# Performance work log

Measured on AMD Instinct MI355X. Metric: run time of the kernel, lower is better.

The kernel has to match this reference:

```python
import jax, jax.numpy as jnp
import numpy as np

K = 20          # n_neighbors
EPS = 1e-5      # batchnorm eps
SLOPE = 0.2     # leaky relu slope (DGCNN default)


def _bn_lrelu(x, axes):
    # batch-norm (per-batch stats, gamma=1, beta=0) + LeakyReLU(0.2)
    m = jnp.mean(x, axis=axes, keepdims=True)
    v = jnp.var(x, axis=axes, keepdims=True)
    return jax.nn.leaky_relu((x - m) * jax.lax.rsqrt(v + EPS), SLOPE)


def _knn(x_cf, k):
    # x_cf: (B, C, N) -> idx (B, N, k) of k nearest neighbors (incl. self)
    inner = jnp.einsum('bcn,bcm->bnm', x_cf, x_cf)
    sq = jnp.sum(x_cf * x_cf, axis=1)                  # (B, N)
    neg_d = 2.0 * inner - sq[:, :, None] - sq[:, None, :]
    return jax.lax.top_k(neg_d, k)[1]


def _gather(x_nl, idx):
    # x_nl: (B, N, C), idx: (B, N, k) -> (B, N, k, C) neighbor features
    return jnp.take_along_axis(x_nl[:, :, None, :], idx[..., None], axis=1)


def setup_inputs() -> dict:
    key = jax.random.key(0)
    ks = jax.random.split(key, 11)
    B, N, C = 16, 2048, 3
    dims = [64, 64, 128, 256]
    feat_dim = 1024

    def w(k, o, i):
        return jax.random.normal(k, (o, i), jnp.float32) / np.sqrt(i)

    return {
        'x': jax.random.normal(ks[0], (B, N, C), jnp.float32),
        'w_edge': w(ks[1], dims[0], 2 * C),
        'b_edge': jnp.zeros((dims[0],), jnp.float32),
        'w1': w(ks[2], dims[1], dims[0]),
        'b1': jnp.zeros((dims[1],), jnp.float32),
        'w2': w(ks[3], dims[2], dims[1]),
        'b2': jnp.zeros((dims[2],), jnp.float32),
        'w3': w(ks[4], dims[3], dims[2]),
        'b3': jnp.zeros((dims[3],), jnp.float32),
        'w_final': w(ks[5], feat_dim, sum(dims)),
        'b_final': jnp.zeros((feat_dim,), jnp.float32),
    }


def reference(x, w_edge, b_edge, w1, b1, w2, b2, w3, b3, w_final, b_final):
    # x: (B, N, 3) point cloud
    x_cf = jnp.transpose(x, (0, 2, 1))                 # (B, 3, N)
    idx = _knn(x_cf, K)                                # (B, N, k) -- graph built once

    # get_graph_features: edge feature = concat(neighbor - center, center)
    nb = _gather(x, idx)                               # (B, N, k, 3)
    ctr = jnp.broadcast_to(x[:, :, None, :], nb.shape)
    feat = jnp.concatenate([nb - ctr, ctr], axis=-1)   # (B, N, k, 6)

    # EdgeConvLayer: 1x1 conv2d + BN + LeakyReLU, then max over neighbors
    h = jnp.einsum('oc,bnkc->bonk', w_edge, feat) + b_edge[None, :, None, None]
    h = _bn_lrelu(h, (0, 2, 3))
    h = jnp.max(h, axis=3)                             # (B, 64, N)

    xs = [h]
    for w, b in ((w1, b1), (w2, b2), (w3, b3)):
        # graph_max_pooling with reused kNN indices
        g = jnp.max(_gather(jnp.transpose(h, (0, 2, 1)), idx), axis=2)  # (B, N, C)
        h = jnp.einsum('oc,bnc->bon', w, g) + b[None, :, None]          # 1x1 conv1d
        h = _bn_lrelu(h, (0, 2))
        xs.append(h)

    h_cat = jnp.concatenate(xs, axis=1)                # (B, 512, N)
    out = jnp.einsum('oc,bcn->bon', w_final, h_cat) + b_final[None, :, None]
    return jnp.max(out, axis=2)                        # (B, 1024)
```

## Files before the change

### kernel.cpp

```cpp
#include <hip/hip_runtime.h>
#include <hip/hip_bf16.h>
#include <math.h>

#define B_ 16
#define N_ 2048
#define KNN 20
#define SLOPE 0.2f
#define EPS_ 1e-5f

#define SEG 8
#define SEGLEN (N_ / SEG)
#define QPB 64
#define CAP 64

typedef __attribute__((ext_vector_type(8))) short short8;
typedef __attribute__((ext_vector_type(4))) float float4v;

__global__ __launch_bounds__(256, 2) void knn_kernel(const float* __restrict__ x,
                                                     int* __restrict__ idx) {
    __shared__ float4 pts4[N_];
    __shared__ float thr[QPB * 24];
    __shared__ float tq[QPB];
    __shared__ int cnt[QPB];
    __shared__ float lv[QPB * CAP];
    __shared__ int   li[QPB * CAP];

    const int b = blockIdx.x >> 5;
    const int qb = blockIdx.x & 31;
    const float* xb = x + (size_t)b * N_ * 3;
    for (int i = threadIdx.x; i < N_; i += 256) {
        float xv = xb[i * 3], yv = xb[i * 3 + 1], zv = xb[i * 3 + 2];
        pts4[i] = make_float4(xv, yv, zv, xv * xv + yv * yv + zv * zv);
    }
    if (threadIdx.x < QPB) cnt[threadIdx.x] = 0;
    __syncthreads();

    const int s = threadIdx.x >> 5;
    const int qs = threadIdx.x & 31;
    const int q0 = qs * 2, q1 = q0 + 1;
    const int n0 = qb * QPB + q0;
    const float4 pa = pts4[n0];
    const float4 pb = pts4[n0 + 1];
    const int m0 = s * SEGLEN;
    const int rot = s * 9;

    float ca[8], cb[8];
#pragma unroll
    for (int c = 0; c < 8; ++c) {
        float va = -INFINITY, vb = -INFINITY;
        for (int i = 0; i < 32; ++i) {
            const int m = m0 + ((c * 32 + i + rot) & (SEGLEN - 1));
            const float4 p = pts4[m];
            va = fmaxf(va, 2.f * (pa.x * p.x + pa.y * p.y + pa.z * p.z) - pa.w - p.w);
            vb = fmaxf(vb, 2.f * (pb.x * p.x + pb.y * p.y + pb.z * p.z) - pb.w - p.w);
        }
        ca[c] = va; cb[c] = vb;
    }
    {
        float t0 = -INFINITY, t1 = -INFINITY, t2 = -INFINITY;
        float u0 = -INFINITY, u1 = -INFINITY, u2 = -INFINITY;
#pragma unroll
        for (int c = 0; c < 8; ++c) {
            float v = ca[c];
            float r0 = fminf(t0, v); t0 = fmaxf(t0, v);
            float r1 = fminf(t1, r0); t1 = fmaxf(t1, r0);
            t2 = fmaxf(t2, r1);
            float w = cb[c];
            float s0 = fminf(u0, w); u0 = fmaxf(u0, w);
            float s1 = fminf(u1, s0); u1 = fmaxf(u1, s0);
            u2 = fmaxf(u2, s1);
        }
        thr[q0 * 24 + s * 3 + 0] = t0;
        thr[q0 * 24 + s * 3 + 1] = t1;
        thr[q0 * 24 + s * 3 + 2] = t2;
        thr[q1 * 24 + s * 3 + 0] = u0;
        thr[q1 * 24 + s * 3 + 1] = u1;
        thr[q1 * 24 + s * 3 + 2] = u2;
    }
    __syncthreads();

    if (threadIdx.x < QPB) {
        const int qq = threadIdx.x;
        float s0 = INFINITY, s1 = INFINITY, s2 = INFINITY, s3 = INFINITY, s4 = INFINITY;
#pragma unroll
        for (int j = 0; j < 24; ++j) {
            float c = thr[qq * 24 + j];
            float u;
            u = fminf(s0, c); c = fmaxf(s0, c); s0 = u;
            u = fminf(s1, c); c = fmaxf(s1, c); s1 = u;
            u = fminf(s2, c); c = fmaxf(s2, c); s2 = u;
            u = fminf(s3, c); c = fmaxf(s3, c); s3 = u;
            s4 = fminf(s4, c);
        }
        tq[qq] = s4 - (fabsf(s4) * 1e-6f + 1e-6f);
    }
    __syncthreads();

    const float ta = tq[q0];
    const float tb = tq[q1];
    for (int i = 0; i < SEGLEN; ++i) {
        const int m = m0 + ((i + rot) & (SEGLEN - 1));
        const float4 p = pts4[m];
        const float da = 2.f * (pa.x * p.x + pa.y * p.y + pa.z * p.z) - pa.w - p.w;
        const float db = 2.f * (pb.x * p.x + pb.y * p.y + pb.z * p.z) - pb.w - p.w;
        if (da >= ta) {
            int pos = atomicAdd(&cnt[q0], 1);
            if (pos < CAP) { lv[q0 * CAP + pos] = da; li[q0 * CAP + pos] = m; }
        }
        if (db >= tb) {
            int pos = atomicAdd(&cnt[q1], 1);
            if (pos < CAP) { lv[q1 * CAP + pos] = db; li[q1 * CAP + pos] = m; }
        }
    }
    __syncthreads();

    if (threadIdx.x < QPB) {
        const int qq = threadIdx.x;
        const int nn = qb * QPB + qq;
        int* op = idx + (size_t)(b * N_ + nn) * KNN;
        float vals[KNN]; int inds[KNN];
#pragma unroll
        for (int j = 0; j < KNN; ++j) { vals[j] = -INFINITY; inds[j] = 0; }
        const int c = cnt[qq];
        if (c <= CAP) {
            for (int j = 0; j < c; ++j) {
                const float v = lv[qq * CAP + j];
                if (v > vals[KNN - 1]) {
                    float cv = v; int ci = li[qq * CAP + j];
#pragma unroll
                    for (int k = 0; k < KNN; ++k) {
                        const bool sw = cv > vals[k];
                        const float tv = vals[k]; const int ti = inds[k];
                        vals[k] = sw ? cv : tv;  inds[k] = sw ? ci : ti;
                        cv      = sw ? tv : cv;  ci      = sw ? ti : ci;
                    }
                }
            }
        } else {
            const float4 pq2 = pts4[nn];
            for (int m = 0; m < N_; ++m) {
                const float4 p = pts4[m];
                const float d = 2.f * (pq2.x * p.x + pq2.y * p.y + pq2.z * p.z)
                                - pq2.w - p.w;
                if (d > vals[KNN - 1]) {
                    float cv = d; int ci = m;
#pragma unroll
                    for (int k = 0; k < KNN; ++k) {
                        const bool sw = cv > vals[k];
                        const float tv = vals[k]; const int ti = inds[k];
                        vals[k] = sw ? cv : tv;  inds[k] = sw ? ci : ti;
                        cv      = sw ? tv : cv;  ci      = sw ? ti : ci;
                    }
                }
            }
        }
#pragma unroll
        for (int j = 0; j < KNN; ++j) op[j] = inds[j];
    }
}

__global__ __launch_bounds__(256) void edge_kernel(const float* __restrict__ x,
                                                   const int* __restrict__ idx,
                                                   const float* __restrict__ w_edge,
                                                   const float* __restrict__ b_edge,
                                                   float* __restrict__ cat,
                                                   double* __restrict__ stats) {
    __shared__ float xs[N_ * 3];
    __shared__ float ws[64 * 6];
    __shared__ float bs[64];
    __shared__ float s_sum[64], s_sq[64];

    int b = blockIdx.x >> 5;
    int pb = blockIdx.x & 31;
    const float* xb = x + (size_t)b * N_ * 3;
    for (int i = threadIdx.x; i < N_ * 3; i += 256) xs[i] = xb[i];
    for (int i = threadIdx.x; i < 64 * 6; i += 256) ws[i] = w_edge[i];
    if (threadIdx.x < 64) {
        bs[threadIdx.x] = b_edge[threadIdx.x];
        s_sum[threadIdx.x] = 0.f; s_sq[threadIdx.x] = 0.f;
    }
    __syncthreads();

    int p = threadIdx.x >> 2;
    int cg = threadIdx.x & 3;
    int n = pb * 64 + p;
    float cx = xs[n * 3], cy = xs[n * 3 + 1], cz = xs[n * 3 + 2];

    float maxv[16], sum[16], sq[16];
#pragma unroll
    for (int i = 0; i < 16; ++i) { maxv[i] = -INFINITY; sum[i] = 0.f; sq[i] = 0.f; }

    const int* ip = idx + (size_t)(b * N_ + n) * KNN;
    for (int k = 0; k < KNN; ++k) {
        int j = ip[k];
        float dx = xs[j * 3] - cx, dy = xs[j * 3 + 1] - cy, dz = xs[j * 3 + 2] - cz;
#pragma unroll
        for (int i = 0; i < 16; ++i) {
            int o = cg * 16 + i;
            const float* wr = &ws[o * 6];
            float h = bs[o] + wr[0] * dx + wr[1] * dy + wr[2] * dz
                            + wr[3] * cx + wr[4] * cy + wr[5] * cz;
            sum[i] += h; sq[i] += h * h;
            maxv[i] = fmaxf(maxv[i], h);
        }
    }

    float* cp = cat + (size_t)(b * N_ + n) * 512;
#pragma unroll
    for (int i = 0; i < 16; ++i) {
        int o = cg * 16 + i;
        cp[o] = maxv[i];
        atomicAdd(&s_sum[o], sum[i]);
        atomicAdd(&s_sq[o], sq[i]);
    }
    __syncthreads();
    if (threadIdx.x < 64) {
        atomicAdd(&stats[threadIdx.x], (double)s_sum[threadIdx.x]);
        atomicAdd(&stats[64 + threadIdx.x], (double)s_sq[threadIdx.x]);
    }
}

__global__ __launch_bounds__(256) void bn_kernel(float* __restrict__ cat,
                                                 __hip_bfloat16* __restrict__ catb,
                                                 const double* __restrict__ stats,
                                                 int C, int off, double invcnt) {
    int t = blockIdx.x * 256 + threadIdx.x;
    int c = t % C;
    int pn = t / C;
    double meand = stats[c] * invcnt;
    double ex2 = stats[C + c] * invcnt;
    float var = (float)(ex2 - meand * meand);
    float mean = (float)meand;
    float inv = rsqrtf(var + EPS_);
    size_t o = (size_t)pn * 512 + off + c;
    float v = (cat[o] - mean) * inv;
    v = v >= 0.f ? v : SLOPE * v;
    cat[o] = v;
    if (catb) catb[o] = __float2bfloat16(v);
}

__global__ __launch_bounds__(256) void wconv_kernel(const float* __restrict__ w,
                                                    __hip_bfloat16* __restrict__ wb) {
    int t = blockIdx.x * 256 + threadIdx.x;
    wb[t] = __float2bfloat16(w[t]);
}

template <int CIN, int COUT, int P, int PT>
__global__ __launch_bounds__(256) void layer_kernel(float* __restrict__ cat,
                                                    const int* __restrict__ idx,
                                                    const float* __restrict__ w,
                                                    const float* __restrict__ bias,
                                                    double* __restrict__ stats,
                                                    int off_in, int off_out) {
    constexpr int LDC = CIN + 4;
    constexpr int WS = COUT + 4;
    constexpr int NCG = CIN / 4;
    constexpr int PPAR = 256 / NCG;
    constexpr int NOG = COUT / 4;

    __shared__ float g[P * LDC];
    __shared__ float wt[16 * WS];
    __shared__ float s_sum[COUT], s_sq[COUT];

    const int pt0 = blockIdx.x * P;
    const int b = pt0 / N_;

    {
        const int cg = threadIdx.x % NCG;
        const int pp = threadIdx.x / NCG;
        for (int p = pp; p < P; p += PPAR) {
            const int* ip = idx + (size_t)(pt0 + p) * KNN;
            float4 m = make_float4(-INFINITY, -INFINITY, -INFINITY, -INFINITY);
#pragma unroll
            for (int k = 0; k < KNN; ++k) {
                const int j = ip[k];
                const float4 v = *(const float4*)&cat[(size_t)(b * N_ + j) * 512 + off_in + cg * 4];
                m.x = fmaxf(m.x, v.x); m.y = fmaxf(m.y, v.y);
                m.z = fmaxf(m.z, v.z); m.w = fmaxf(m.w, v.w);
            }
            *(float4*)&g[p * LDC + cg * 4] = m;
        }
    }
    if (threadIdx.x < COUT) { s_sum[threadIdx.x] = 0.f; s_sq[threadIdx.x] = 0.f; }

    const int og = threadIdx.x % NOG;
    const int pg = threadIdx.x / NOG;
    const int o0 = og * 4, p0 = pg * PT;

    float acc[4][PT];
#pragma unroll
    for (int i = 0; i < 4; ++i)
#pragma unroll
        for (int j = 0; j < PT; ++j) acc[i][j] = 0.f;

    for (int c0 = 0; c0 < CIN; c0 += 16) {
        __syncthreads();
        for (int i = threadIdx.x; i < COUT * 16; i += 256) {
            int o = i >> 4, cc = i & 15;
            wt[cc * WS + o] = w[(size_t)o * CIN + c0 + cc];
        }
        __syncthreads();
#pragma unroll
        for (int cc = 0; cc < 16; ++cc) {
            const float4 wv = *(const float4*)&wt[cc * WS + o0];
            const float* gp = &g[p0 * LDC + c0 + cc];
#pragma unroll
            for (int p = 0; p < PT; ++p) {
                const float gv = gp[p * LDC];
                acc[0][p] += wv.x * gv;
                acc[1][p] += wv.y * gv;
                acc[2][p] += wv.z * gv;
                acc[3][p] += wv.w * gv;
            }
        }
    }

    const float4 bv = *(const float4*)&bias[o0];
    float lsum[4] = {0.f, 0.f, 0.f, 0.f}, lsq[4] = {0.f, 0.f, 0.f, 0.f};
#pragma unroll
    for (int p = 0; p < PT; ++p) {
        float4 hv;
        hv.x = acc[0][p] + bv.x; hv.y = acc[1][p] + bv.y;
        hv.z = acc[2][p] + bv.z; hv.w = acc[3][p] + bv.w;
        lsum[0] += hv.x; lsq[0] += hv.x * hv.x;
        lsum[1] += hv.y; lsq[1] += hv.y * hv.y;
        lsum[2] += hv.z; lsq[2] += hv.z * hv.z;
        lsum[3] += hv.w; lsq[3] += hv.w * hv.w;
        *(float4*)&cat[(size_t)(pt0 + p0 + p) * 512 + off_out + o0] = hv;
    }
#pragma unroll
    for (int i = 0; i < 4; ++i) {
        atomicAdd(&s_sum[o0 + i], lsum[i]);
        atomicAdd(&s_sq[o0 + i], lsq[i]);
    }
    __syncthreads();
    if (threadIdx.x < COUT) {
        atomicAdd(&stats[threadIdx.x], (double)s_sum[threadIdx.x]);
        atomicAdd(&stats[COUT + threadIdx.x], (double)s_sq[threadIdx.x]);
    }
}

__global__ __launch_bounds__(256) void final_mfma_kernel(const short* __restrict__ catb,
                                                         const short* __restrict__ wb,
                                                         const float* __restrict__ bias,
                                                         float* __restrict__ partial) {
    constexpr int LDK = 72;
    __shared__ short As[128 * LDK];
    __shared__ short Bs[128 * LDK];
    __shared__ float red[256];

    const int ob = blockIdx.x;
    const int pblk = blockIdx.y;
    const int pt0 = pblk * 128;

    const int wid = threadIdx.x >> 6;
    const int lane = threadIdx.x & 63;
    const int wm = wid >> 1, wn = wid & 1;
    const int lm = lane & 15, g = lane >> 4;

    const int srow = threadIdx.x >> 1;
    const int scg = (threadIdx.x & 1) * 32;
    const short* ga = catb + (size_t)(pt0 + srow) * 512 + scg;
    const short* gb = wb + (size_t)(ob * 128 + srow) * 512 + scg;
    short* la = As + srow * LDK + scg;
    short* lb = Bs + srow * LDK + scg;

    float4v acc[4][4];
#pragma unroll
    for (int i = 0; i < 4; ++i)
#pragma unroll
        for (int j = 0; j < 4; ++j) acc[i][j] = {0.f, 0.f, 0.f, 0.f};

    short8 ra[4], rb[4];
#pragma unroll
    for (int j = 0; j < 4; ++j) {
        ra[j] = *(const short8*)(ga + j * 8);
        rb[j] = *(const short8*)(gb + j * 8);
    }

    for (int step = 0; step < 8; ++step) {
        __syncthreads();
#pragma unroll
        for (int j = 0; j < 4; ++j) {
            *(short8*)(la + j * 8) = ra[j];
            *(short8*)(lb + j * 8) = rb[j];
        }
        __syncthreads();
        if (step < 7) {
            const int c1 = (step + 1) * 64;
#pragma unroll
            for (int j = 0; j < 4; ++j) {
                ra[j] = *(const short8*)(ga + c1 + j * 8);
                rb[j] = *(const short8*)(gb + c1 + j * 8);
            }
        }
#pragma unroll
        for (int kk = 0; kk < 2; ++kk) {
            short8 a[4], b[4];
#pragma unroll
            for (int t = 0; t < 4; ++t) {
                a[t] = *(const short8*)&As[(wm * 64 + t * 16 + lm) * LDK + kk * 32 + g * 8];
                b[t] = *(const short8*)&Bs[(wn * 64 + t * 16 + lm) * LDK + kk * 32 + g * 8];
            }
#pragma unroll
            for (int mt = 0; mt < 4; ++mt)
#pragma unroll
                for (int nt = 0; nt < 4; ++nt)
                    acc[mt][nt] = __builtin_amdgcn_mfma_f32_16x16x32_bf16(
                        a[mt], b[nt], acc[mt][nt], 0, 0, 0);
        }
    }

    float cm[4];
#pragma unroll
    for (int nt = 0; nt < 4; ++nt) {
        float m = -INFINITY;
#pragma unroll
        for (int mt = 0; mt < 4; ++mt)
#pragma unroll
            for (int r = 0; r < 4; ++r) m = fmaxf(m, acc[mt][nt][r]);
        m = fmaxf(m, __shfl_xor(m, 16, 64));
        m = fmaxf(m, __shfl_xor(m, 32, 64));
        cm[nt] = m;
    }
    __syncthreads();
    if (lane < 16) {
#pragma unroll
        for (int nt = 0; nt < 4; ++nt)
            red[wm * 128 + wn * 64 + nt * 16 + lane] = cm[nt];
    }
    __syncthreads();
    if (threadIdx.x < 128) {
        const int o = threadIdx.x;
        float v = fmaxf(red[o], red[128 + o]) + bias[ob * 128 + o];
        partial[(size_t)pblk * 1024 + ob * 128 + o] = v;
    }
}

__global__ __launch_bounds__(256) void final_kernel(const float* __restrict__ cat,
                                                    const float* __restrict__ w,
                                                    const float* __restrict__ bias,
                                                    float* __restrict__ partial) {
    __shared__ float As[16 * 132];
    __shared__ float Ws[16 * 132];
    __shared__ float red[16 * 128];

    const int ob = blockIdx.x;
    const int pblk = blockIdx.y;
    const int pt0 = pblk * 128;
    const int tx = threadIdx.x & 15;
    const int ty = threadIdx.x >> 4;

    float acc[8][8];
#pragma unroll
    for (int i = 0; i < 8; ++i)
#pragma unroll
        for (int j = 0; j < 8; ++j) acc[i][j] = 0.f;

    const int row = threadIdx.x & 127;
    const int half = threadIdx.x >> 7;
    const float* arow = cat + (size_t)(pt0 + row) * 512 + half * 8;
    const float* wrow = w + (size_t)(ob * 128 + row) * 512 + half * 8;

    for (int c0 = 0; c0 < 512; c0 += 16) {
        __syncthreads();
        float4 v0 = *(const float4*)(arow + c0);
        float4 v1 = *(const float4*)(arow + c0 + 4);
        float4 u0 = *(const float4*)(wrow + c0);
        float4 u1 = *(const float4*)(wrow + c0 + 4);
        const int cb = half * 8;
        As[(cb + 0) * 132 + row] = v0.x; As[(cb + 1) * 132 + row] = v0.y;
        As[(cb + 2) * 132 + row] = v0.z; As[(cb + 3) * 132 + row] = v0.w;
        As[(cb + 4) * 132 + row] = v1.x; As[(cb + 5) * 132 + row] = v1.y;
        As[(cb + 6) * 132 + row] = v1.z; As[(cb + 7) * 132 + row] = v1.w;
        Ws[(cb + 0) * 132 + row] = u0.x; Ws[(cb + 1) * 132 + row] = u0.y;
        Ws[(cb + 2) * 132 + row] = u0.z; Ws[(cb + 3) * 132 + row] = u0.w;
        Ws[(cb + 4) * 132 + row] = u1.x; Ws[(cb + 5) * 132 + row] = u1.y;
        Ws[(cb + 6) * 132 + row] = u1.z; Ws[(cb + 7) * 132 + row] = u1.w;
        __syncthreads();
#pragma unroll
        for (int cc = 0; cc < 16; ++cc) {
            const float4* Ap = (const float4*)(As + cc * 132);
            const float4* Wp = (const float4*)(Ws + cc * 132);
            float4 a0 = Ap[ty], a1 = Ap[ty + 16];
            float4 w0 = Wp[tx], w1 = Wp[tx + 16];
            float av[8] = {a0.x, a0.y, a0.z, a0.w, a1.x, a1.y, a1.z, a1.w};
            float wv[8] = {w0.x, w0.y, w0.z, w0.w, w1.x, w1.y, w1.z, w1.w};
#pragma unroll
            for (int i = 0; i < 8; ++i)
#pragma unroll
                for (int j = 0; j < 8; ++j)
                    acc[i][j] += av[i] * wv[j];
        }
    }

#pragma unroll
    for (int j = 0; j < 8; ++j) {
        float mm = acc[0][j];
#pragma unroll
        for (int i = 1; i < 8; ++i) mm = fmaxf(mm, acc[i][j]);
        const int o = (j < 4) ? tx * 4 + j : 64 + tx * 4 + (j - 4);
        red[ty * 128 + o] = mm;
    }
    __syncthreads();
    if (threadIdx.x < 128) {
        const int o = threadIdx.x;
        float mm = red[o];
#pragma unroll
        for (int r = 1; r < 16; ++r) mm = fmaxf(mm, red[r * 128 + o]);
        partial[(size_t)pblk * 1024 + ob * 128 + o] = mm + bias[ob * 128 + o];
    }
}

__global__ __launch_bounds__(256) void reduce_kernel(const float* __restrict__ partial,
                                                     float* __restrict__ out) {
    int t = blockIdx.x * 256 + threadIdx.x;
    int b = t >> 10, o = t & 1023;
    float m = -INFINITY;
#pragma unroll 4
    for (int i = 0; i < 16; ++i)
        m = fmaxf(m, partial[(size_t)((b * 16 + i) * 1024) + o]);
    out[t] = m;
}

extern "C" void kernel_launch(void* const* d_in, const int* in_sizes, int n_in,
                              void* d_out, int out_size, void* d_ws, size_t ws_size,
                              hipStream_t stream) {
    const float* x = (const float*)d_in[0];
    const float* w_edge = (const float*)d_in[1];
    const float* b_edge = (const float*)d_in[2];
    const float* w1 = (const float*)d_in[3];
    const float* b1 = (const float*)d_in[4];
    const float* w2 = (const float*)d_in[5];
    const float* b2 = (const float*)d_in[6];
    const float* w3 = (const float*)d_in[7];
    const float* b3 = (const float*)d_in[8];
    const float* w_final = (const float*)d_in[9];
    const float* b_final = (const float*)d_in[10];
    float* out = (float*)d_out;

    char* ws = (char*)d_ws;
    int* idx = (int*)ws;
    float* cat = (float*)(ws + 2621440);
    float* partial = (float*)(ws + 69730304);
    double* stats = (double*)(ws + 70778880);
    __hip_bfloat16* catb = (__hip_bfloat16*)(ws + 70787072);
    __hip_bfloat16* wb = (__hip_bfloat16*)(ws + 104341504);
    const size_t WS_NEED = 105390080;
    const bool use_mfma = (ws_size >= WS_NEED);
    __hip_bfloat16* catb_arg = use_mfma ? catb : (__hip_bfloat16*)0;

    double* st_e = stats;
    double* st_1 = stats + 128;
    double* st_2 = stats + 256;
    double* st_3 = stats + 512;

    hipMemsetAsync(stats, 0, 1024 * sizeof(double), stream);
    if (use_mfma)
        wconv_kernel<<<2048, 256, 0, stream>>>(w_final, wb);

    knn_kernel<<<B_ * 32, 256, 0, stream>>>(x, idx);
    edge_kernel<<<B_ * 32, 256, 0, stream>>>(x, idx, w_edge, b_edge, cat, st_e);
    bn_kernel<<<(B_ * N_ * 64) / 256, 256, 0, stream>>>(cat, catb_arg, st_e, 64, 0,
                                                        1.0 / ((double)B_ * N_ * KNN));
    layer_kernel<64, 64, 64, 4><<<(B_ * N_) / 64, 256, 0, stream>>>(cat, idx, w1, b1, st_1, 0, 64);
    bn_kernel<<<(B_ * N_ * 64) / 256, 256, 0, stream>>>(cat, catb_arg, st_1, 64, 64,
                                                        1.0 / ((double)B_ * N_));
    layer_kernel<64, 128, 64, 8><<<(B_ * N_) / 64, 256, 0, stream>>>(cat, idx, w2, b2, st_2, 64, 128);
    bn_kernel<<<(B_ * N_ * 128) / 256, 256, 0, stream>>>(cat, catb_arg, st_2, 128, 128,
                                                         1.0 / ((double)B_ * N_));
    layer_kernel<128, 256, 64, 16><<<(B_ * N_) / 64, 256, 0, stream>>>(cat, idx, w3, b3, st_3, 128, 256);
    bn_kernel<<<(B_ * N_ * 256) / 256, 256, 0, stream>>>(cat, catb_arg, st_3, 256, 256,
                                                         1.0 / ((double)B_ * N_));
    if (use_mfma)
        final_mfma_kernel<<<dim3(8, 256), 256, 0, stream>>>((const short*)catb, (const short*)wb,
                                                            b_final, partial);
    else
        final_kernel<<<dim3(8, 256), 256, 0, stream>>>(cat, w_final, b_final, partial);
    reduce_kernel<<<64, 256, 0, stream>>>(partial, out);
}
```

Before: 437.3 us.

## Fuse BN+LeakyReLU into neighbor gather and consolidate BN into single bf16 pass

Removes the four separate bn_kernel passes. Each layer now applies the previous layer's batch-norm and LeakyReLU while it gathers and max-pools neighbor features. This is valid because the transform is monotonic per channel, so it commutes with max. A single bnconv_kernel then normalizes the whole 512-channel concat buffer to bf16 for the MFMA final GEMM. It also changes the layer's weight smem layout to per-output rows with float4 reads over input channels, drops the rotated scan order in kNN, and removes the fp32 fallback final kernel. The goal is to cut global read/write traffic and launch count, at the cost of a workspace-size check and possible LDS bank conflicts.

```diff
diff --git a/kernel.cpp b/kernel.cpp
--- a/kernel.cpp
+++ b/kernel.cpp
@@ -42,14 +42,13 @@
     const float4 pa = pts4[n0];
     const float4 pb = pts4[n0 + 1];
     const int m0 = s * SEGLEN;
-    const int rot = s * 9;
 
     float ca[8], cb[8];
 #pragma unroll
     for (int c = 0; c < 8; ++c) {
         float va = -INFINITY, vb = -INFINITY;
         for (int i = 0; i < 32; ++i) {
-            const int m = m0 + ((c * 32 + i + rot) & (SEGLEN - 1));
+            const int m = m0 + c * 32 + i;
             const float4 p = pts4[m];
             va = fmaxf(va, 2.f * (pa.x * p.x + pa.y * p.y + pa.z * p.z) - pa.w - p.w);
             vb = fmaxf(vb, 2.f * (pb.x * p.x + pb.y * p.y + pb.z * p.z) - pb.w - p.w);
@@ -99,7 +98,7 @@
     const float ta = tq[q0];
     const float tb = tq[q1];
     for (int i = 0; i < SEGLEN; ++i) {
-        const int m = m0 + ((i + rot) & (SEGLEN - 1));
+        const int m = m0 + i;
         const float4 p = pts4[m];
         const float da = 2.f * (pa.x * p.x + pa.y * p.y + pa.z * p.z) - pa.w - p.w;
         const float db = 2.f * (pb.x * p.x + pb.y * p.y + pb.z * p.z) - pb.w - p.w;
@@ -220,46 +219,30 @@
     }
 }
 
-__global__ __launch_bounds__(256) void bn_kernel(float* __restrict__ cat,
-                                                 __hip_bfloat16* __restrict__ catb,
-                                                 const double* __restrict__ stats,
-                                                 int C, int off, double invcnt) {
-    int t = blockIdx.x * 256 + threadIdx.x;
-    int c = t % C;
-    int pn = t / C;
-    double meand = stats[c] * invcnt;
-    double ex2 = stats[C + c] * invcnt;
-    float var = (float)(ex2 - meand * meand);
-    float mean = (float)meand;
-    float inv = rsqrtf(var + EPS_);
-    size_t o = (size_t)pn * 512 + off + c;
-    float v = (cat[o] - mean) * inv;
-    v = v >= 0.f ? v : SLOPE * v;
-    cat[o] = v;
-    if (catb) catb[o] = __float2bfloat16(v);
-}
-
 __global__ __launch_bounds__(256) void wconv_kernel(const float* __restrict__ w,
                                                     __hip_bfloat16* __restrict__ wb) {
     int t = blockIdx.x * 256 + threadIdx.x;
     wb[t] = __float2bfloat16(w[t]);
 }
 
-template <int CIN, int COUT, int P, int PT>
+template <int CIN, int COUT, int PT>
 __global__ __launch_bounds__(256) void layer_kernel(float* __restrict__ cat,
                                                     const int* __restrict__ idx,
                                                     const float* __restrict__ w,
                                                     const float* __restrict__ bias,
-                                                    double* __restrict__ stats,
+                                                    const double* __restrict__ stats_in,
+                                                    double invcnt_in,
+                                                    double* __restrict__ stats_out,
                                                     int off_in, int off_out) {
+    constexpr int P = 64;
     constexpr int LDC = CIN + 4;
-    constexpr int WS = COUT + 4;
     constexpr int NCG = CIN / 4;
     constexpr int PPAR = 256 / NCG;
     constexpr int NOG = COUT / 4;
+    static_assert(NOG * (P / PT) == 256, "thread mapping");
 
     __shared__ float g[P * LDC];
-    __shared__ float wt[16 * WS];
+    __shared__ float wt[COUT * 20];
     __shared__ float s_sum[COUT], s_sq[COUT];
 
     const int pt0 = blockIdx.x * P;
@@ -268,6 +251,15 @@
     {
         const int cg = threadIdx.x % NCG;
         const int pp = threadIdx.x / NCG;
+        float mean[4], inv[4];
+#pragma unroll
+        for (int j = 0; j < 4; ++j) {
+            const double mu = stats_in[cg * 4 + j] * invcnt_in;
+            const double e2 = stats_in[CIN + cg * 4 + j] * invcnt_in;
+            const float var = (float)(e2 - mu * mu);
+            mean[j] = (float)mu;
+            inv[j] = rsqrtf(var + EPS_);
+        }
         for (int p = pp; p < P; p += PPAR) {
             const int* ip = idx + (size_t)(pt0 + p) * KNN;
             float4 m = make_float4(-INFINITY, -INFINITY, -INFINITY, -INFINITY);
@@ -278,7 +270,12 @@
                 m.x = fmaxf(m.x, v.x); m.y = fmaxf(m.y, v.y);
                 m.z = fmaxf(m.z, v.z); m.w = fmaxf(m.w, v.w);
             }
-            *(float4*)&g[p * LDC + cg * 4] = m;
+            float4 r;
+            r.x = (m.x - mean[0]) * inv[0]; r.x = r.x >= 0.f ? r.x : SLOPE * r.x;
+            r.y = (m.y - mean[1]) * inv[1]; r.y = r.y >= 0.f ? r.y : SLOPE * r.y;
+            r.z = (m.z - mean[2]) * inv[2]; r.z = r.z >= 0.f ? r.z : SLOPE * r.z;
+            r.w = (m.w - mean[3]) * inv[3]; r.w = r.w >= 0.f ? r.w : SLOPE * r.w;
+            *(float4*)&g[p * LDC + cg * 4] = r;
         }
     }
     if (threadIdx.x < COUT) { s_sum[threadIdx.x] = 0.f; s_sq[threadIdx.x] = 0.f; }
@@ -297,20 +294,26 @@
         __syncthreads();
         for (int i = threadIdx.x; i < COUT * 16; i += 256) {
             int o = i >> 4, cc = i & 15;
-            wt[cc * WS + o] = w[(size_t)o * CIN + c0 + cc];
+            wt[o * 20 + cc] = w[(size_t)o * CIN + c0 + cc];
         }
         __syncthreads();
 #pragma unroll
-        for (int cc = 0; cc < 16; ++cc) {
-            const float4 wv = *(const float4*)&wt[cc * WS + o0];
-            const float* gp = &g[p0 * LDC + c0 + cc];
+        for (int ccq = 0; ccq < 4; ++ccq) {
+            const float4 w0 = *(const float4*)&wt[(o0 + 0) * 20 + ccq * 4];
+            const float4 w1 = *(const float4*)&wt[(o0 + 1) * 20 + ccq * 4];
+            const float4 w2 = *(const float4*)&wt[(o0 + 2) * 20 + ccq * 4];
+            const float4 w3 = *(const float4*)&wt[(o0 + 3) * 20 + ccq * 4];
 #pragma unroll
             for (int p = 0; p < PT; ++p) {
-                const float gv = gp[p * LDC];
-                acc[0][p] += wv.x * gv;
-                acc[1][p] += wv.y * gv;
-                acc[2][p] += wv.z * gv;
-                acc[3][p] += wv.w * gv;
+                const float4 gv = *(const float4*)&g[(p0 + p) * LDC + c0 + ccq * 4];
+                acc[0][p] += w0.x * gv.x; acc[0][p] += w0.y * gv.y;
+                acc[0][p] += w0.z * gv.z; acc[0][p] += w0.w * gv.w;
+                acc[1][p] += w1.x * gv.x; acc[1][p] += w1.y * gv.y;
+                acc[1][p] += w1.z * gv.z; acc[1][p] += w1.w * gv.w;
+                acc[2][p] += w2.x * gv.x; acc[2][p] += w2.y * gv.y;
+                acc[2][p] += w2.z * gv.z; acc[2][p] += w2.w * gv.w;
+                acc[3][p] += w3.x * gv.x; acc[3][p] += w3.y * gv.y;
+                acc[3][p] += w3.z * gv.z; acc[3][p] += w3.w * gv.w;
             }
         }
     }
@@ -335,9 +338,42 @@
     }
     __syncthreads();
     if (threadIdx.x < COUT) {
-        atomicAdd(&stats[threadIdx.x], (double)s_sum[threadIdx.x]);
-        atomicAdd(&stats[COUT + threadIdx.x], (double)s_sq[threadIdx.x]);
-    }
+        atomicAdd(&stats_out[threadIdx.x], (double)s_sum[threadIdx.x]);
+        atomicAdd(&stats_out[COUT + threadIdx.x], (double)s_sq[threadIdx.x]);
+    }
+}
+
+__global__ __launch_bounds__(256) void bnconv_kernel(const float* __restrict__ cat,
+                                                     const double* __restrict__ stats,
+                                                     unsigned short* __restrict__ catb,
+                                                     double ik, double in_) {
+    const int t = blockIdx.x * 256 + threadIdx.x;
+    const int pn = t >> 7;
+    const int c = (t & 127) * 4;
+
+    const double* sp; const double* qp; double icnt;
+    if (c < 64)       { sp = stats + c;             qp = stats + 64 + c;        icnt = ik; }
+    else if (c < 128) { sp = stats + 128 + (c - 64);  qp = stats + 192 + (c - 64);  icnt = in_; }
+    else if (c < 256) { sp = stats + 256 + (c - 128); qp = stats + 384 + (c - 128); icnt = in_; }
+    else              { sp = stats + 512 + (c - 256); qp = stats + 768 + (c - 256); icnt = in_; }
+
+    const float4 v = *(const float4*)&cat[(size_t)pn * 512 + c];
+    float r[4]; const float vv[4] = {v.x, v.y, v.z, v.w};
+#pragma unroll
+    for (int j = 0; j < 4; ++j) {
+        const double mu = sp[j] * icnt;
+        const double e2 = qp[j] * icnt;
+        const float var = (float)(e2 - mu * mu);
+        const float inv = rsqrtf(var + EPS_);
+        float x = (vv[j] - (float)mu) * inv;
+        r[j] = x >= 0.f ? x : SLOPE * x;
+    }
+    ushort4 o;
+    __hip_bfloat16 h0 = __float2bfloat16(r[0]); o.x = *(unsigned short*)&h0;
+    __hip_bfloat16 h1 = __float2bfloat16(r[1]); o.y = *(unsigned short*)&h1;
+    __hip_bfloat16 h2 = __float2bfloat16(r[2]); o.z = *(unsigned short*)&h2;
+    __hip_bfloat16 h3 = __float2bfloat16(r[3]); o.w = *(unsigned short*)&h3;
+    *(ushort4*)&catb[(size_t)pn * 512 + c] = o;
 }
 
 __global__ __launch_bounds__(256) void final_mfma_kernel(const short* __restrict__ catb,
@@ -434,81 +470,6 @@
         const int o = threadIdx.x;
         float v = fmaxf(red[o], red[128 + o]) + bias[ob * 128 + o];
         partial[(size_t)pblk * 1024 + ob * 128 + o] = v;
-    }
-}
-
-__global__ __launch_bounds__(256) void final_kernel(const float* __restrict__ cat,
-                                                    const float* __restrict__ w,
-                                                    const float* __restrict__ bias,
-                                                    float* __restrict__ partial) {
-    __shared__ float As[16 * 132];
-    __shared__ float Ws[16 * 132];
-    __shared__ float red[16 * 128];
-
-    const int ob = blockIdx.x;
-    const int pblk = blockIdx.y;
-    const int pt0 = pblk * 128;
-    const int tx = threadIdx.x & 15;
-    const int ty = threadIdx.x >> 4;
-
-    float acc[8][8];
-#pragma unroll
-    for (int i = 0; i < 8; ++i)
-#pragma unroll
-        for (int j = 0; j < 8; ++j) acc[i][j] = 0.f;
-
-    const int row = threadIdx.x & 127;
-    const int half = threadIdx.x >> 7;
-    const float* arow = cat + (size_t)(pt0 + row) * 512 + half * 8;
-    const float* wrow = w + (size_t)(ob * 128 + row) * 512 + half * 8;
-
-    for (int c0 = 0; c0 < 512; c0 += 16) {
-        __syncthreads();
-        float4 v0 = *(const float4*)(arow + c0);
-        float4 v1 = *(const float4*)(arow + c0 + 4);
-        float4 u0 = *(const float4*)(wrow + c0);
-        float4 u1 = *(const float4*)(wrow + c0 + 4);
-        const int cb = half * 8;
-        As[(cb + 0) * 132 + row] = v0.x; As[(cb + 1) * 132 + row] = v0.y;
-        As[(cb + 2) * 132 + row] = v0.z; As[(cb + 3) * 132 + row] = v0.w;
-        As[(cb + 4) * 132 + row] = v1.x; As[(cb + 5) * 132 + row] = v1.y;
-        As[(cb + 6) * 132 + row] = v1.z; As[(cb + 7) * 132 + row] = v1.w;
-        Ws[(cb + 0) * 132 + row] = u0.x; Ws[(cb + 1) * 132 + row] = u0.y;
-        Ws[(cb + 2) * 132 + row] = u0.z; Ws[(cb + 3) * 132 + row] = u0.w;
-        Ws[(cb + 4) * 132 + row] = u1.x; Ws[(cb + 5) * 132 + row] = u1.y;
-        Ws[(cb + 6) * 132 + row] = u1.z; Ws[(cb + 7) * 132 + row] = u1.w;
-        __syncthreads();
-#pragma unroll
-        for (int cc = 0; cc < 16; ++cc) {
-            const float4* Ap = (const float4*)(As + cc * 132);
-            const float4* Wp = (const float4*)(Ws + cc * 132);
-            float4 a0 = Ap[ty], a1 = Ap[ty + 16];
-            float4 w0 = Wp[tx], w1 = Wp[tx + 16];
-            float av[8] = {a0.x, a0.y, a0.z, a0.w, a1.x, a1.y, a1.z, a1.w};
-            float wv[8] = {w0.x, w0.y, w0.z, w0.w, w1.x, w1.y, w1.z, w1.w};
-#pragma unroll
-            for (int i = 0; i < 8; ++i)
-#pragma unroll
-                for (int j = 0; j < 8; ++j)
-                    acc[i][j] += av[i] * wv[j];
-        }
-    }
-
-#pragma unroll
-    for (int j = 0; j < 8; ++j) {
-        float mm = acc[0][j];
-#pragma unroll
-        for (int i = 1; i < 8; ++i) mm = fmaxf(mm, acc[i][j]);
-        const int o = (j < 4) ? tx * 4 + j : 64 + tx * 4 + (j - 4);
-        red[ty * 128 + o] = mm;
-    }
-    __syncthreads();
-    if (threadIdx.x < 128) {
-        const int o = threadIdx.x;
-        float mm = red[o];
-#pragma unroll
-        for (int r = 1; r < 16; ++r) mm = fmaxf(mm, red[r * 128 + o]);
-        partial[(size_t)pblk * 1024 + ob * 128 + o] = mm + bias[ob * 128 + o];
     }
 }
 
@@ -546,36 +507,28 @@
     double* stats = (double*)(ws + 70778880);
     __hip_bfloat16* catb = (__hip_bfloat16*)(ws + 70787072);
     __hip_bfloat16* wb = (__hip_bfloat16*)(ws + 104341504);
-    const size_t WS_NEED = 105390080;
-    const bool use_mfma = (ws_size >= WS_NEED);
-    __hip_bfloat16* catb_arg = use_mfma ? catb : (__hip_bfloat16*)0;
 
     double* st_e = stats;
     double* st_1 = stats + 128;
     double* st_2 = stats + 256;
     double* st_3 = stats + 512;
+    const double ik = 1.0 / ((double)B_ * N_ * KNN);
+    const double in_ = 1.0 / ((double)B_ * N_);
 
     hipMemsetAsync(stats, 0, 1024 * sizeof(double), stream);
-    if (use_mfma)
-        wconv_kernel<<<2048, 256, 0, stream>>>(w_final, wb);
+    wconv_kernel<<<2048, 256, 0, stream>>>(w_final, wb);
 
     knn_kernel<<<B_ * 32, 256, 0, stream>>>(x, idx);
     edge_kernel<<<B_ * 32, 256, 0, stream>>>(x, idx, w_edge, b_edge, cat, st_e);
-    bn_kernel<<<(B_ * N_ * 64) / 256, 256, 0, stream>>>(cat, catb_arg, st_e, 64, 0,
-                                                        1.0 / ((double)B_ * N_ * KNN));
-    layer_kernel<64, 64, 64, 4><<<(B_ * N_) / 64, 256, 0, stream>>>(cat, idx, w1, b1, st_1, 0, 64);
-    bn_kernel<<<(B_ * N_ * 64) / 256, 256, 0, stream>>>(cat, catb_arg, st_1, 64, 64,
-                                                        1.0 / ((double)B_ * N_));
-    layer_kernel<64, 128, 64, 8><<<(B_ * N_) / 64, 256, 0, stream>>>(cat, idx, w2, b2, st_2, 64, 128);
-    bn_kernel<<<(B_ * N_ * 128) / 256, 256, 0, stream>>>(cat, catb_arg, st_2, 128, 128,
-                                                         1.0 / ((double)B_ * N_));
-    layer_kernel<128, 256, 64, 16><<<(B_ * N_) / 64, 256, 0, stream>>>(cat, idx, w3, b3, st_3, 128, 256);
-    bn_kernel<<<(B_ * N_ * 256) / 256, 256, 0, stream>>>(cat, catb_arg, st_3, 256, 256,
-                                                         1.0 / ((double)B_ * N_));
-    if (use_mfma)
-        final_mfma_kernel<<<dim3(8, 256), 256, 0, stream>>>((const short*)catb, (const short*)wb,
-                                                            b_final, partial);
-    else
-        final_kernel<<<dim3(8, 256), 256, 0, stream>>>(cat, w_final, b_final, partial);
+    layer_kernel<64, 64, 4><<<(B_ * N_) / 64, 256, 0, stream>>>(
+        cat, idx, w1, b1, st_e, ik, st_1, 0, 64);
+    layer_kernel<64, 128, 8><<<(B_ * N_) / 64, 256, 0, stream>>>(
+        cat, idx, w2, b2, st_1, in_, st_2, 64, 128);
+    layer_kernel<128, 256, 16><<<(B_ * N_) / 64, 256, 0, stream>>>(
+        cat, idx, w3, b3, st_2, in_, st_3, 128, 256);
+    bnconv_kernel<<<(B_ * N_ * 128) / 256, 256, 0, stream>>>(
+        cat, stats, (unsigned short*)catb, ik, in_);
+    final_mfma_kernel<<<dim3(8, 256), 256, 0, stream>>>((const short*)catb, (const short*)wb,
+                                                        b_final, partial);
     reduce_kernel<<<64, 256, 0, stream>>>(partial, out);
 }
```

New measurement: 475.7 us. +8.8%, slower.
